# Optimization experiments

Hardware: AMD Instinct MI355X
Metric: run time of the kernel (lower is better)

The kernel has to match this reference:

```python
import jax, jax.numpy as jnp
import numpy as np

N = 10000       # nodes
E = 320000      # edges (before self-loops)
IN = 16         # in_channels


def _p(key, shape, scale=0.1):
    return jax.random.normal(key, shape, jnp.float32) * scale


def setup_inputs() -> dict:
    key = jax.random.key(0)
    ks = jax.random.split(key, 26)
    d = {}
    d["x"] = jax.random.normal(ks[0], (N, IN), jnp.float32)
    d["edge_index"] = jax.random.randint(ks[1], (2, E), 0, N, jnp.int32)
    d["JetRawPt"] = jax.random.normal(ks[2], (N, 1), jnp.float32)
    # conv1: GATConv(16 -> 32, heads=8)
    d["W1"] = _p(ks[3], (IN, 8 * 32)); d["a1s"] = _p(ks[4], (8, 32)); d["a1d"] = _p(ks[5], (8, 32)); d["b1"] = jnp.zeros((256,), jnp.float32)
    # conv2: GATConv(256 -> 32, heads=8)
    d["W2"] = _p(ks[6], (256, 8 * 32)); d["a2s"] = _p(ks[7], (8, 32)); d["a2d"] = _p(ks[8], (8, 32)); d["b2"] = jnp.zeros((256,), jnp.float32)
    # conv3: GATConv(256 -> 64, heads=12)
    d["W3"] = _p(ks[9], (256, 12 * 64)); d["a3s"] = _p(ks[10], (12, 64)); d["a3d"] = _p(ks[11], (12, 64)); d["b3"] = jnp.zeros((768,), jnp.float32)
    # linear_final: 256+256+768=1280 -> 1
    d["Wf"] = _p(ks[12], (1280, 1)); d["bf"] = jnp.zeros((1,), jnp.float32)
    # MLP: (16+1)->128->64->1
    d["M1w"] = _p(ks[13], (IN + 1, 128)); d["M1b"] = jnp.zeros((128,), jnp.float32)
    d["M2w"] = _p(ks[14], (128, 64)); d["M2b"] = jnp.zeros((64,), jnp.float32)
    d["M3w"] = _p(ks[15], (64, 1)); d["M3b"] = jnp.zeros((1,), jnp.float32)
    return d


def gat_layer(x, src, dst, W, a_s, a_d, b, H, C):
    # PyG GATConv (eval mode, self-loops already appended to src/dst)
    h = (x @ W).reshape(-1, H, C)                      # [N, H, C]
    al = jnp.sum(h * a_s, axis=-1)                     # [N, H] src-side score
    ar = jnp.sum(h * a_d, axis=-1)                     # [N, H] dst-side score
    e = jax.nn.leaky_relu(al[src] + ar[dst], 0.2)      # [Etot, H]
    m = jax.ops.segment_max(e, dst, num_segments=N)    # segment softmax over incoming edges
    ex = jnp.exp(e - m[dst])
    s = jax.ops.segment_sum(ex, dst, num_segments=N)
    alpha = ex / s[dst]                                # [Etot, H]
    out = jax.ops.segment_sum(h[src] * alpha[:, :, None], dst, num_segments=N)  # [N, H, C]
    return out.reshape(-1, H * C) + b


def reference(x, edge_index, JetRawPt, W1, a1s, a1d, b1, W2, a2s, a2d, b2,
              W3, a3s, a3d, b3, Wf, bf, M1w, M1b, M2w, M2b, M3w, M3b):
    loops = jnp.arange(N, dtype=edge_index.dtype)
    src = jnp.concatenate([edge_index[0], loops])
    dst = jnp.concatenate([edge_index[1], loops])
    x1 = jax.nn.relu(gat_layer(x, src, dst, W1, a1s, a1d, b1, 8, 32))
    x2 = jax.nn.relu(gat_layer(x1, src, dst, W2, a2s, a2d, b2, 8, 32))
    x3 = jax.nn.relu(gat_layer(x2, src, dst, W3, a3s, a3d, b3, 12, 64))
    xc = jnp.concatenate([x1, x2, x3], axis=1)         # [N, 1280]
    out1 = jax.nn.sigmoid(xc @ Wf + bf)                # [N, 1]
    xm = jnp.concatenate([x, out1], axis=1)            # [N, 17]
    h = jax.nn.relu(xm @ M1w + M1b)
    h = jax.nn.relu(h @ M2w + M2b)
    out2 = jax.nn.sigmoid(h @ M3w + M3b)               # [N, 1]
    return (out1, out2)
```

## Files before the change

### kernel.cpp

```cpp
#include <hip/hip_runtime.h>
#include <math.h>


typedef unsigned short bf16_t;
typedef __attribute__((ext_vector_type(8))) short bf16x8;
typedef __attribute__((ext_vector_type(4))) float f32x4;

__device__ inline float bf2f(bf16_t u) {
    union { unsigned int i; float f; } v; v.i = ((unsigned int)u) << 16; return v.f;
}
__device__ inline float u2f(unsigned int x) {
    union { unsigned int i; float f; } v; v.i = x; return v.f;
}
__device__ inline bf16_t f2bf(float f) {
    union { float f; unsigned int i; } v; v.f = f;
    unsigned int r = v.i + 0x7FFF + ((v.i >> 16) & 1);
    return (bf16_t)(r >> 16);
}


__global__ void zero_i32(int* p, int n) {
    int i = blockIdx.x * blockDim.x + threadIdx.x;
    if (i < n) p[i] = 0;
}

__global__ void count_edges(const int* __restrict__ ei, int E, int Nn,
                            int* __restrict__ counts) {
    int e = blockIdx.x * blockDim.x + threadIdx.x;
    if (e >= E + Nn) return;
    int dst = (e < E) ? ei[E + e] : (e - E);
    atomicAdd(&counts[dst], 1);
}

__global__ __launch_bounds__(1024) void scan_rowptr(const int* __restrict__ counts,
                                                    int* __restrict__ rowptr, int n) {
    const int IPT = (n + 1023) / 1024;
    int t = threadIdx.x;
    int base = t * IPT;
    int loc[16];
    int run = 0;
#pragma unroll
    for (int i = 0; i < 16; i++) {
        if (i >= IPT) break;
        int idx = base + i;
        int v = (idx < n) ? counts[idx] : 0;
        loc[i] = run;
        run += v;
    }
    int lane = t & 63, wid = t >> 6;
    int v = run;
    for (int off = 1; off < 64; off <<= 1) {
        int u = __shfl_up(v, off, 64);
        if (lane >= off) v += u;
    }
    __shared__ int wsum[16];
    __shared__ int woff[16];
    if (lane == 63) wsum[wid] = v;
    __syncthreads();
    if (t == 0) { int s = 0; for (int i = 0; i < 16; i++) { woff[i] = s; s += wsum[i]; } }
    __syncthreads();
    int excl = v - run + woff[wid];
#pragma unroll
    for (int i = 0; i < 16; i++) {
        if (i >= IPT) break;
        int idx = base + i;
        if (idx < n) rowptr[idx] = excl + loc[i];
    }
    if (t == 1023) rowptr[n] = excl + run;
}

__global__ void fill_edges(const int* __restrict__ ei, int E, int Nn,
                           const int* __restrict__ rowptr, int* __restrict__ cursor,
                           int* __restrict__ edge_src) {
    int e = blockIdx.x * blockDim.x + threadIdx.x;
    if (e >= E + Nn) return;
    int src, dst;
    if (e < E) { src = ei[e]; dst = ei[E + e]; }
    else       { src = e - E; dst = src; }
    int pos = atomicAdd(&cursor[dst], 1);
    edge_src[rowptr[dst] + pos] = src;
}

__global__ __launch_bounds__(256) void transpose_cast2(const float* __restrict__ W2,
                                                       bf16_t* __restrict__ Wt2,
                                                       const float* __restrict__ W3,
                                                       bf16_t* __restrict__ Wt3) {
    __shared__ float tile[16][17];
    const float* W; bf16_t* Wt; int Nc, n0;
    if (blockIdx.y < 16) { W = W2; Wt = Wt2; Nc = 256; n0 = blockIdx.y * 16; }
    else                 { W = W3; Wt = Wt3; Nc = 768; n0 = (blockIdx.y - 16) * 16; }
    int k0 = blockIdx.x * 16;
    int tx = threadIdx.x & 15, ty = threadIdx.x >> 4;
    tile[ty][tx] = W[(size_t)(k0 + ty) * Nc + n0 + tx];
    __syncthreads();
    Wt[(size_t)(n0 + ty) * 256 + k0 + tx] = f2bf(tile[tx][ty]);
}

__global__ __launch_bounds__(256) void gemm_f32_sc(const float* __restrict__ A,
                                                   const float* __restrict__ B,
                                                   bf16_t* __restrict__ Cm,
                                                   const float* __restrict__ a_s,
                                                   const float* __restrict__ a_d,
                                                   float* __restrict__ al,
                                                   float* __restrict__ ar,
                                                   int M, int K, int Nc, int H) {
    __shared__ float As[16][64];
    __shared__ float Bs[16][64];
    int t  = threadIdx.x;
    int tx = t & 15, ty = t >> 4;
    int row0 = blockIdx.y * 64, col0 = blockIdx.x * 64;
    int a_r = t >> 2, a_c = (t & 3) * 4;
    int b_r = t >> 4, b_c = (t & 15) * 4;

    float acc[4][4];
#pragma unroll
    for (int i = 0; i < 4; i++)
#pragma unroll
        for (int j = 0; j < 4; j++) acc[i][j] = 0.f;

    for (int kt = 0; kt < K; kt += 16) {
        float4 av = make_float4(0.f, 0.f, 0.f, 0.f);
        int gr = row0 + a_r;
        if (gr < M) av = *(const float4*)(A + (size_t)gr * K + kt + a_c);
        As[a_c + 0][a_r] = av.x;
        As[a_c + 1][a_r] = av.y;
        As[a_c + 2][a_r] = av.z;
        As[a_c + 3][a_r] = av.w;
        float4 bv = *(const float4*)(B + (size_t)(kt + b_r) * Nc + col0 + b_c);
        *(float4*)&Bs[b_r][b_c] = bv;
        __syncthreads();
#pragma unroll
        for (int k = 0; k < 16; k++) {
            float4 a4 = *(const float4*)&As[k][ty * 4];
            float4 b4 = *(const float4*)&Bs[k][tx * 4];
            float aa[4] = {a4.x, a4.y, a4.z, a4.w};
            float bb[4] = {b4.x, b4.y, b4.z, b4.w};
#pragma unroll
            for (int i = 0; i < 4; i++)
#pragma unroll
                for (int j = 0; j < 4; j++) acc[i][j] += aa[i] * bb[j];
        }
        __syncthreads();
    }
    float4 asv = *(const float4*)(a_s + col0 + tx * 4);
    float4 adv = *(const float4*)(a_d + col0 + tx * 4);
#pragma unroll
    for (int i = 0; i < 4; i++) {
        int gr = row0 + ty * 4 + i;
        float sa = acc[i][0] * asv.x + acc[i][1] * asv.y + acc[i][2] * asv.z + acc[i][3] * asv.w;
        float sd = acc[i][0] * adv.x + acc[i][1] * adv.y + acc[i][2] * adv.z + acc[i][3] * adv.w;
#pragma unroll
        for (int off = 4; off > 0; off >>= 1) {
            sa += __shfl_xor(sa, off, 64);
            sd += __shfl_xor(sd, off, 64);
        }
        if ((tx == 0 || tx == 8) && gr < M) {
            int h = (col0 >> 5) + (tx >> 3);
            al[gr * H + h] = sa;
            ar[gr * H + h] = sd;
        }
        if (gr < M) {
            ushort4 v;
            v.x = f2bf(acc[i][0]); v.y = f2bf(acc[i][1]);
            v.z = f2bf(acc[i][2]); v.w = f2bf(acc[i][3]);
            *(ushort4*)(Cm + (size_t)gr * Nc + col0 + tx * 4) = v;
        }
    }
}

template <int C_>
__global__ __launch_bounds__(256) void gemm_mfma_sc(const bf16_t* __restrict__ A,
                                                    const bf16_t* __restrict__ Bt,
                                                    bf16_t* __restrict__ Cm,
                                                    const float* __restrict__ a_s,
                                                    const float* __restrict__ a_d,
                                                    float* __restrict__ al,
                                                    float* __restrict__ ar,
                                                    int M, int K, int Nc, int H) {
    int wave = threadIdx.x >> 6, lane = threadIdx.x & 63;
    int quad = lane >> 4, l16 = lane & 15;
    int m0 = blockIdx.y * 128 + wave * 32;
    int n0 = blockIdx.x * 64;

    f32x4 acc[2][4];
    f32x4 z = {0.f, 0.f, 0.f, 0.f};
#pragma unroll
    for (int i = 0; i < 2; i++)
#pragma unroll
        for (int j = 0; j < 4; j++) acc[i][j] = z;

    int r0 = m0 + l16;       if (r0 >= M) r0 = M - 1;
    int r1 = m0 + 16 + l16;  if (r1 >= M) r1 = M - 1;
    const bf16_t* Ap0 = A + (size_t)r0 * K + quad * 8;
    const bf16_t* Ap1 = A + (size_t)r1 * K + quad * 8;
    const bf16_t* Bp0 = Bt + (size_t)(n0 + 0  + l16) * K + quad * 8;
    const bf16_t* Bp1 = Bt + (size_t)(n0 + 16 + l16) * K + quad * 8;
    const bf16_t* Bp2 = Bt + (size_t)(n0 + 32 + l16) * K + quad * 8;
    const bf16_t* Bp3 = Bt + (size_t)(n0 + 48 + l16) * K + quad * 8;

    for (int kt = 0; kt < K; kt += 32) {
        bf16x8 a0 = *(const bf16x8*)(Ap0 + kt);
        bf16x8 a1 = *(const bf16x8*)(Ap1 + kt);
        bf16x8 b0 = *(const bf16x8*)(Bp0 + kt);
        bf16x8 b1 = *(const bf16x8*)(Bp1 + kt);
        bf16x8 b2 = *(const bf16x8*)(Bp2 + kt);
        bf16x8 b3 = *(const bf16x8*)(Bp3 + kt);
        acc[0][0] = __builtin_amdgcn_mfma_f32_16x16x32_bf16(a0, b0, acc[0][0], 0, 0, 0);
        acc[1][0] = __builtin_amdgcn_mfma_f32_16x16x32_bf16(a1, b0, acc[1][0], 0, 0, 0);
        acc[0][1] = __builtin_amdgcn_mfma_f32_16x16x32_bf16(a0, b1, acc[0][1], 0, 0, 0);
        acc[1][1] = __builtin_amdgcn_mfma_f32_16x16x32_bf16(a1, b1, acc[1][1], 0, 0, 0);
        acc[0][2] = __builtin_amdgcn_mfma_f32_16x16x32_bf16(a0, b2, acc[0][2], 0, 0, 0);
        acc[1][2] = __builtin_amdgcn_mfma_f32_16x16x32_bf16(a1, b2, acc[1][2], 0, 0, 0);
        acc[0][3] = __builtin_amdgcn_mfma_f32_16x16x32_bf16(a0, b3, acc[0][3], 0, 0, 0);
        acc[1][3] = __builtin_amdgcn_mfma_f32_16x16x32_bf16(a1, b3, acc[1][3], 0, 0, 0);
    }

    float asv[4], adv[4];
#pragma unroll
    for (int j = 0; j < 4; j++) {
        asv[j] = a_s[n0 + j * 16 + l16];
        adv[j] = a_d[n0 + j * 16 + l16];
    }
#pragma unroll
    for (int i = 0; i < 2; i++)
#pragma unroll
        for (int r = 0; r < 4; r++) {
            int gr = m0 + i * 16 + quad * 4 + r;
            if (C_ == 64) {
                float sa = acc[i][0][r] * asv[0] + acc[i][1][r] * asv[1]
                         + acc[i][2][r] * asv[2] + acc[i][3][r] * asv[3];
                float sd = acc[i][0][r] * adv[0] + acc[i][1][r] * adv[1]
                         + acc[i][2][r] * adv[2] + acc[i][3][r] * adv[3];
#pragma unroll
                for (int off = 8; off > 0; off >>= 1) {
                    sa += __shfl_xor(sa, off, 64);
                    sd += __shfl_xor(sd, off, 64);
                }
                if (l16 == 0 && gr < M) {
                    int h = n0 >> 6;
                    al[gr * H + h] = sa;
                    ar[gr * H + h] = sd;
                }
            } else {
                float saA = acc[i][0][r] * asv[0] + acc[i][1][r] * asv[1];
                float saB = acc[i][2][r] * asv[2] + acc[i][3][r] * asv[3];
                float sdA = acc[i][0][r] * adv[0] + acc[i][1][r] * adv[1];
                float sdB = acc[i][2][r] * adv[2] + acc[i][3][r] * adv[3];
#pragma unroll
                for (int off = 8; off > 0; off >>= 1) {
                    saA += __shfl_xor(saA, off, 64);
                    saB += __shfl_xor(saB, off, 64);
                    sdA += __shfl_xor(sdA, off, 64);
                    sdB += __shfl_xor(sdB, off, 64);
                }
                if (l16 == 0 && gr < M) {
                    int h = n0 >> 5;
                    al[gr * H + h]     = saA;
                    ar[gr * H + h]     = sdA;
                    al[gr * H + h + 1] = saB;
                    ar[gr * H + h + 1] = sdB;
                }
            }
        }
#pragma unroll
    for (int i = 0; i < 2; i++)
#pragma unroll
        for (int j = 0; j < 4; j++)
#pragma unroll
            for (int r = 0; r < 4; r++) {
                int gr = m0 + i * 16 + quad * 4 + r;
                if (gr < M) Cm[(size_t)gr * Nc + n0 + j * 16 + l16] = f2bf(acc[i][j][r]);
            }
}

template <int H>
__global__ __launch_bounds__(256) void alpha_node(const float* __restrict__ al,
                                                  const float* __restrict__ ar,
                                                  const int* __restrict__ rowptr,
                                                  const int* __restrict__ esrc,
                                                  float* __restrict__ alpha,
                                                  int n, int Etot) {
    int node = (blockIdx.x * blockDim.x + threadIdx.x) >> 6;
    if (node >= n) return;
    int lane = threadIdx.x & 63;

    float arv[H];
#pragma unroll
    for (int h4 = 0; h4 < H; h4 += 4) {
        float4 t = *(const float4*)(ar + (size_t)node * H + h4);
        arv[h4] = t.x; arv[h4 + 1] = t.y; arv[h4 + 2] = t.z; arv[h4 + 3] = t.w;
    }
    int beg = rowptr[node], end = rowptr[node + 1];
    float p0[H], p1[H], s[H];
#pragma unroll
    for (int h = 0; h < H; h++) { p0[h] = 0.f; p1[h] = 0.f; s[h] = 0.f; }

    int j0 = beg + lane;
    if (j0 < end) {
        const float* alr = al + (size_t)esrc[j0] * H;
#pragma unroll
        for (int h4 = 0; h4 < H; h4 += 4) {
            float4 t = *(const float4*)(alr + h4);
            float e;
            e = t.x + arv[h4];     e = fmaxf(e, 0.2f * e); p0[h4]     = __expf(fminf(e, 60.f));
            e = t.y + arv[h4 + 1]; e = fmaxf(e, 0.2f * e); p0[h4 + 1] = __expf(fminf(e, 60.f));
            e = t.z + arv[h4 + 2]; e = fmaxf(e, 0.2f * e); p0[h4 + 2] = __expf(fminf(e, 60.f));
            e = t.w + arv[h4 + 3]; e = fmaxf(e, 0.2f * e); p0[h4 + 3] = __expf(fminf(e, 60.f));
        }
#pragma unroll
        for (int h = 0; h < H; h++) s[h] += p0[h];
    }
    int j1 = j0 + 64;
    if (j1 < end) {
        const float* alr = al + (size_t)esrc[j1] * H;
#pragma unroll
        for (int h4 = 0; h4 < H; h4 += 4) {
            float4 t = *(const float4*)(alr + h4);
            float e;
            e = t.x + arv[h4];     e = fmaxf(e, 0.2f * e); p1[h4]     = __expf(fminf(e, 60.f));
            e = t.y + arv[h4 + 1]; e = fmaxf(e, 0.2f * e); p1[h4 + 1] = __expf(fminf(e, 60.f));
            e = t.z + arv[h4 + 2]; e = fmaxf(e, 0.2f * e); p1[h4 + 2] = __expf(fminf(e, 60.f));
            e = t.w + arv[h4 + 3]; e = fmaxf(e, 0.2f * e); p1[h4 + 3] = __expf(fminf(e, 60.f));
        }
#pragma unroll
        for (int h = 0; h < H; h++) s[h] += p1[h];
    }
    for (int j = j0 + 128; j < end; j += 64) {
        const float* alr = al + (size_t)esrc[j] * H;
#pragma unroll
        for (int h = 0; h < H; h++) {
            float e = alr[h] + arv[h];
            e = fmaxf(e, 0.2f * e);
            float p = __expf(fminf(e, 60.f));
            alpha[(size_t)h * Etot + j] = p;
            s[h] += p;
        }
    }
#pragma unroll
    for (int h = 0; h < H; h++) {
        float v = s[h];
#pragma unroll
        for (int off = 32; off > 0; off >>= 1) v += __shfl_xor(v, off, 64);
        s[h] = 1.f / v;
    }
    if (j0 < end) {
#pragma unroll
        for (int h = 0; h < H; h++) alpha[(size_t)h * Etot + j0] = p0[h] * s[h];
    }
    if (j1 < end) {
#pragma unroll
        for (int h = 0; h < H; h++) alpha[(size_t)h * Etot + j1] = p1[h] * s[h];
    }
    for (int j = j0 + 128; j < end; j += 64) {
#pragma unroll
        for (int h = 0; h < H; h++) alpha[(size_t)h * Etot + j] *= s[h];
    }
}

template <int HC_, int C>
__global__ __launch_bounds__(256) void gat_agg(
    const bf16_t* __restrict__ hbuf, const float* __restrict__ alpha,
    const int* __restrict__ rowptr, const int* __restrict__ esrc,
    const float* __restrict__ bias, bf16_t* __restrict__ outb,
    int n, int Etot, int nodeblocks) {
    int group = blockIdx.x / nodeblocks;
    int nb    = blockIdx.x - group * nodeblocks;
    int node  = nb * 4 + (threadIdx.x >> 6);
    if (node >= n) return;
    int lane = threadIdx.x & 63;
    int sub  = lane >> 4;
    int cl   = lane & 15;
    int gc   = group * 128 + cl * 8;
    int head = gc / C;
    const bf16_t* hb = hbuf + gc;
    const float*  ap = alpha + (size_t)head * Etot;

    float acc[8];
#pragma unroll
    for (int i = 0; i < 8; i++) acc[i] = 0.f;

    int beg = rowptr[node], end = rowptr[node + 1];
    int deg = end - beg;

    int e0 = 0, e1 = 0;
    {
        int i0 = beg + lane;
        if (i0 < end) e0 = esrc[i0];
        int i1 = beg + 64 + lane;
        if (i1 < end) e1 = esrc[i1];
    }
    int npre  = deg < 128 ? deg : 128;
    int nfull = npre >> 3;

    if (nfull > 0) {
        int s0 = __shfl(e0, sub, 64);
        int s1 = __shfl(e0, sub + 4, 64);
        float a0 = ap[beg + sub], a1 = ap[beg + sub + 4];
        bf16x8 u0 = *(const bf16x8*)(hb + (size_t)s0 * HC_);
        bf16x8 u1 = *(const bf16x8*)(hb + (size_t)s1 * HC_);
        for (int it = 1; it < nfull; ++it) {
            int kb = it * 8;
            int esel = (kb < 64) ? e0 : e1;
            int t0 = __shfl(esel, (kb + sub) & 63, 64);
            int t1 = __shfl(esel, (kb + sub + 4) & 63, 64);
            float b0v = ap[beg + kb + sub], b1v = ap[beg + kb + sub + 4];
            bf16x8 v0 = *(const bf16x8*)(hb + (size_t)t0 * HC_);
            bf16x8 v1 = *(const bf16x8*)(hb + (size_t)t1 * HC_);
            const unsigned int* d0 = (const unsigned int*)&u0;
            const unsigned int* d1 = (const unsigned int*)&u1;
#pragma unroll
            for (int i = 0; i < 4; i++) {
                acc[2 * i]     += a0 * u2f(d0[i] << 16);
                acc[2 * i + 1] += a0 * u2f(d0[i] & 0xffff0000u);
                acc[2 * i]     += a1 * u2f(d1[i] << 16);
                acc[2 * i + 1] += a1 * u2f(d1[i] & 0xffff0000u);
            }
            u0 = v0; u1 = v1; a0 = b0v; a1 = b1v;
        }
        const unsigned int* d0 = (const unsigned int*)&u0;
        const unsigned int* d1 = (const unsigned int*)&u1;
#pragma unroll
        for (int i = 0; i < 4; i++) {
            acc[2 * i]     += a0 * u2f(d0[i] << 16);
            acc[2 * i + 1] += a0 * u2f(d0[i] & 0xffff0000u);
            acc[2 * i]     += a1 * u2f(d1[i] << 16);
            acc[2 * i + 1] += a1 * u2f(d1[i] & 0xffff0000u);
        }
    }
    for (int j = beg + (nfull << 3) + sub; j < end; j += 4) {
        int s0 = esrc[j];
        float a0 = ap[j];
        bf16x8 u0 = *(const bf16x8*)(hb + (size_t)s0 * HC_);
        const unsigned int* d0 = (const unsigned int*)&u0;
#pragma unroll
        for (int i = 0; i < 4; i++) {
            acc[2 * i]     += a0 * u2f(d0[i] << 16);
            acc[2 * i + 1] += a0 * u2f(d0[i] & 0xffff0000u);
        }
    }
#pragma unroll
    for (int i = 0; i < 8; i++) {
        acc[i] += __shfl_xor(acc[i], 16, 64);
        acc[i] += __shfl_xor(acc[i], 32, 64);
    }
    if (sub == 0) {
        float4 b0 = *(const float4*)(bias + gc);
        float4 b1 = *(const float4*)(bias + gc + 4);
        float bb[8] = {b0.x, b0.y, b0.z, b0.w, b1.x, b1.y, b1.z, b1.w};
        bf16x8 outv;
        unsigned short* ov = (unsigned short*)&outv;
#pragma unroll
        for (int i = 0; i < 8; i++) ov[i] = f2bf(fmaxf(acc[i] + bb[i], 0.f));
        *(bf16x8*)(outb + (size_t)node * HC_ + gc) = outv;
    }
}

__global__ __launch_bounds__(256) void head_fused(
    const float* __restrict__ x, const bf16_t* __restrict__ x1b,
    const bf16_t* __restrict__ x2b, const bf16_t* __restrict__ x3b,
    const float* __restrict__ Wf, const float* __restrict__ bfc,
    const float* __restrict__ M1w, const float* __restrict__ M1b,
    const float* __restrict__ M2w, const float* __restrict__ M2b,
    const float* __restrict__ M3w, const float* __restrict__ M3b,
    float* __restrict__ out1, float* __restrict__ out2, int n) {
    __shared__ float h1s[4][128];
    int w    = threadIdx.x >> 6;
    int lane = threadIdx.x & 63;
    int node = blockIdx.x * 4 + w;
    bool valid = node < n;
    int nd = valid ? node : 0;

    float s = 0.f;
    {
        ushort4 u = *(const ushort4*)(x1b + (size_t)nd * 256 + lane * 4);
        const float* wv = Wf + lane * 4;
        s += bf2f(u.x) * wv[0] + bf2f(u.y) * wv[1] + bf2f(u.z) * wv[2] + bf2f(u.w) * wv[3];
    }
    {
        ushort4 u = *(const ushort4*)(x2b + (size_t)nd * 256 + lane * 4);
        const float* wv = Wf + 256 + lane * 4;
        s += bf2f(u.x) * wv[0] + bf2f(u.y) * wv[1] + bf2f(u.z) * wv[2] + bf2f(u.w) * wv[3];
    }
#pragma unroll
    for (int i = 0; i < 3; i++) {
        int k = i * 256 + lane * 4;
        ushort4 u = *(const ushort4*)(x3b + (size_t)nd * 768 + k);
        const float* wv = Wf + 512 + k;
        s += bf2f(u.x) * wv[0] + bf2f(u.y) * wv[1] + bf2f(u.z) * wv[2] + bf2f(u.w) * wv[3];
    }
#pragma unroll
    for (int off = 32; off > 0; off >>= 1) s += __shfl_xor(s, off, 64);
    float so = 1.f / (1.f + __expf(-(s + bfc[0])));
    if (lane == 0 && valid) out1[node] = so;

    float xm[17];
#pragma unroll
    for (int k = 0; k < 16; k++) xm[k] = x[nd * 16 + k];
    xm[16] = so;

    float a0 = M1b[lane], a1 = M1b[lane + 64];
#pragma unroll
    for (int k = 0; k < 17; k++) {
        a0 += xm[k] * M1w[k * 128 + lane];
        a1 += xm[k] * M1w[k * 128 + lane + 64];
    }
    h1s[w][lane]      = fmaxf(a0, 0.f);
    h1s[w][lane + 64] = fmaxf(a1, 0.f);
    __syncthreads();

    float b0 = M2b[lane];
#pragma unroll 16
    for (int k = 0; k < 128; k++) b0 += h1s[w][k] * M2w[k * 64 + lane];
    b0 = fmaxf(b0, 0.f);

    float p = b0 * M3w[lane];
#pragma unroll
    for (int off = 32; off > 0; off >>= 1) p += __shfl_xor(p, off, 64);
    if (lane == 0 && valid) out2[node] = 1.f / (1.f + __expf(-(p + M3b[0])));
}

extern "C" void kernel_launch(void* const* d_in, const int* in_sizes, int n_in,
                              void* d_out, int out_size, void* d_ws, size_t ws_size,
                              hipStream_t stream) {
    const float* x   = (const float*)d_in[0];
    const int*   ei  = (const int*)d_in[1];
    const float* W1  = (const float*)d_in[3];
    const float* a1s = (const float*)d_in[4];
    const float* a1d = (const float*)d_in[5];
    const float* b1  = (const float*)d_in[6];
    const float* W2  = (const float*)d_in[7];
    const float* a2s = (const float*)d_in[8];
    const float* a2d = (const float*)d_in[9];
    const float* b2  = (const float*)d_in[10];
    const float* W3  = (const float*)d_in[11];
    const float* a3s = (const float*)d_in[12];
    const float* a3d = (const float*)d_in[13];
    const float* b3  = (const float*)d_in[14];
    const float* Wf  = (const float*)d_in[15];
    const float* bf  = (const float*)d_in[16];
    const float* M1w = (const float*)d_in[17];
    const float* M1b = (const float*)d_in[18];
    const float* M2w = (const float*)d_in[19];
    const float* M2b = (const float*)d_in[20];
    const float* M3w = (const float*)d_in[21];
    const float* M3b = (const float*)d_in[22];

    const int N = in_sizes[0] / 16;
    const int E = in_sizes[1] / 2;
    const int Etot = E + N;

    char* base = (char*)d_ws;
    size_t off = 0;
    auto carve = [&](size_t bytes) {
        char* p = base + off;
        off = (off + bytes + 255) & ~(size_t)255;
        return p;
    };
    bf16_t* hbuf   = (bf16_t*)carve((size_t)N * 768 * 2);
    bf16_t* x1b    = (bf16_t*)carve((size_t)N * 256 * 2);
    bf16_t* x2b    = (bf16_t*)carve((size_t)N * 256 * 2);
    bf16_t* x3b    = (bf16_t*)carve((size_t)N * 768 * 2);
    bf16_t* Wt2    = (bf16_t*)carve((size_t)256 * 256 * 2);
    bf16_t* Wt3    = (bf16_t*)carve((size_t)256 * 768 * 2);
    float*  al     = (float*)carve((size_t)N * 12 * 4);
    float*  ar     = (float*)carve((size_t)N * 12 * 4);
    float*  alphab = (float*)carve((size_t)Etot * 12 * 4);
    int*    rowptr = (int*)carve((size_t)(N + 1) * 4);
    int*    cnt2   = (int*)carve((size_t)(2 * N) * 4);
    int*    counts = cnt2;
    int*    cursor = cnt2 + N;
    int*    esrc   = (int*)carve((size_t)Etot * 4);
    (void)ws_size;

    float* out1 = (float*)d_out;
    float* out2 = (float*)d_out + N;

    const int TB = 256;
    int eb = (Etot + TB - 1) / TB;
    int nodeblocks = (N + 3) / 4;

    zero_i32<<<(2 * N + TB - 1) / TB, TB, 0, stream>>>(cnt2, 2 * N);
    count_edges<<<eb, TB, 0, stream>>>(ei, E, N, counts);
    scan_rowptr<<<1, 1024, 0, stream>>>(counts, rowptr, N);
    fill_edges<<<eb, TB, 0, stream>>>(ei, E, N, rowptr, cursor, esrc);
    transpose_cast2<<<dim3(16, 64), TB, 0, stream>>>(W2, Wt2, W3, Wt3);

    gemm_f32_sc<<<dim3(4, (N + 63) / 64), TB, 0, stream>>>(x, W1, hbuf, a1s, a1d, al, ar, N, 16, 256, 8);
    alpha_node<8><<<nodeblocks, TB, 0, stream>>>(al, ar, rowptr, esrc, alphab, N, Etot);
    gat_agg<256, 32><<<2 * nodeblocks, TB, 0, stream>>>(hbuf, alphab, rowptr, esrc, b1, x1b, N, Etot, nodeblocks);

    gemm_mfma_sc<32><<<dim3(4, (N + 127) / 128), TB, 0, stream>>>(x1b, Wt2, hbuf, a2s, a2d, al, ar, N, 256, 256, 8);
    alpha_node<8><<<nodeblocks, TB, 0, stream>>>(al, ar, rowptr, esrc, alphab, N, Etot);
    gat_agg<256, 32><<<2 * nodeblocks, TB, 0, stream>>>(hbuf, alphab, rowptr, esrc, b2, x2b, N, Etot, nodeblocks);

    gemm_mfma_sc<64><<<dim3(12, (N + 127) / 128), TB, 0, stream>>>(x2b, Wt3, hbuf, a3s, a3d, al, ar, N, 256, 768, 12);
    alpha_node<12><<<nodeblocks, TB, 0, stream>>>(al, ar, rowptr, esrc, alphab, N, Etot);
    gat_agg<768, 64><<<6 * nodeblocks, TB, 0, stream>>>(hbuf, alphab, rowptr, esrc, b3, x3b, N, Etot, nodeblocks);

    head_fused<<<nodeblocks, TB, 0, stream>>>(x, x1b, x2b, x3b, Wf, bf,
                                              M1w, M1b, M2w, M2b, M3w, M3b, out1, out2, N);
}
```

Baseline: 335.1 us.

## Process two nodes per wavefront in alpha_node, pack aggregation FMAs, use memset

alpha_node now gives each node a 32-lane half wavefront instead of a full 64-lane wavefront. With about 33 edges per node, this cuts idle lanes and halves the grid, though high-degree nodes now loop more. gat_agg accumulates into float2 vectors, aiming for packed FP32 FMA instructions. The zero-fill kernel is replaced by hipMemsetAsync.

```diff
diff --git a/kernel.cpp b/kernel.cpp
--- a/kernel.cpp
+++ b/kernel.cpp
@@ -5,6 +5,7 @@
 typedef unsigned short bf16_t;
 typedef __attribute__((ext_vector_type(8))) short bf16x8;
 typedef __attribute__((ext_vector_type(4))) float f32x4;
+typedef __attribute__((ext_vector_type(2))) float f32x2;
 
 __device__ inline float bf2f(bf16_t u) {
     union { unsigned int i; float f; } v; v.i = ((unsigned int)u) << 16; return v.f;
@@ -18,11 +19,6 @@
     return (bf16_t)(r >> 16);
 }
 
-
-__global__ void zero_i32(int* p, int n) {
-    int i = blockIdx.x * blockDim.x + threadIdx.x;
-    if (i < n) p[i] = 0;
-}
 
 __global__ void count_edges(const int* __restrict__ ei, int E, int Nn,
                             int* __restrict__ counts) {
@@ -280,9 +276,11 @@
                                                   const int* __restrict__ esrc,
                                                   float* __restrict__ alpha,
                                                   int n, int Etot) {
-    int node = (blockIdx.x * blockDim.x + threadIdx.x) >> 6;
+    int pair = (blockIdx.x * blockDim.x + threadIdx.x) >> 6;
+    int lane = threadIdx.x & 63;
+    int node = pair * 2 + (lane >> 5);
     if (node >= n) return;
-    int lane = threadIdx.x & 63;
+    int lane32 = lane & 31;
 
     float arv[H];
 #pragma unroll
@@ -295,7 +293,7 @@
 #pragma unroll
     for (int h = 0; h < H; h++) { p0[h] = 0.f; p1[h] = 0.f; s[h] = 0.f; }
 
-    int j0 = beg + lane;
+    int j0 = beg + lane32;
     if (j0 < end) {
         const float* alr = al + (size_t)esrc[j0] * H;
 #pragma unroll
@@ -310,7 +308,7 @@
 #pragma unroll
         for (int h = 0; h < H; h++) s[h] += p0[h];
     }
-    int j1 = j0 + 64;
+    int j1 = j0 + 32;
     if (j1 < end) {
         const float* alr = al + (size_t)esrc[j1] * H;
 #pragma unroll
@@ -325,7 +323,7 @@
 #pragma unroll
         for (int h = 0; h < H; h++) s[h] += p1[h];
     }
-    for (int j = j0 + 128; j < end; j += 64) {
+    for (int j = j0 + 64; j < end; j += 32) {
         const float* alr = al + (size_t)esrc[j] * H;
 #pragma unroll
         for (int h = 0; h < H; h++) {
@@ -340,7 +338,7 @@
     for (int h = 0; h < H; h++) {
         float v = s[h];
 #pragma unroll
-        for (int off = 32; off > 0; off >>= 1) v += __shfl_xor(v, off, 64);
+        for (int off = 16; off > 0; off >>= 1) v += __shfl_xor(v, off, 64);
         s[h] = 1.f / v;
     }
     if (j0 < end) {
@@ -351,7 +349,7 @@
 #pragma unroll
         for (int h = 0; h < H; h++) alpha[(size_t)h * Etot + j1] = p1[h] * s[h];
     }
-    for (int j = j0 + 128; j < end; j += 64) {
+    for (int j = j0 + 64; j < end; j += 32) {
 #pragma unroll
         for (int h = 0; h < H; h++) alpha[(size_t)h * Etot + j] *= s[h];
     }
@@ -375,9 +373,10 @@
     const bf16_t* hb = hbuf + gc;
     const float*  ap = alpha + (size_t)head * Etot;
 
-    float acc[8];
-#pragma unroll
-    for (int i = 0; i < 8; i++) acc[i] = 0.f;
+    f32x2 acc2[4];
+    f32x2 z2 = {0.f, 0.f};
+#pragma unroll
+    for (int i = 0; i < 4; i++) acc2[i] = z2;
 
     int beg = rowptr[node], end = rowptr[node + 1];
     int deg = end - beg;
@@ -408,23 +407,25 @@
             bf16x8 v1 = *(const bf16x8*)(hb + (size_t)t1 * HC_);
             const unsigned int* d0 = (const unsigned int*)&u0;
             const unsigned int* d1 = (const unsigned int*)&u1;
+            f32x2 a0v = {a0, a0}, a1v = {a1, a1};
 #pragma unroll
             for (int i = 0; i < 4; i++) {
-                acc[2 * i]     += a0 * u2f(d0[i] << 16);
-                acc[2 * i + 1] += a0 * u2f(d0[i] & 0xffff0000u);
-                acc[2 * i]     += a1 * u2f(d1[i] << 16);
-                acc[2 * i + 1] += a1 * u2f(d1[i] & 0xffff0000u);
+                f32x2 w0 = {u2f(d0[i] << 16), u2f(d0[i] & 0xffff0000u)};
+                f32x2 w1 = {u2f(d1[i] << 16), u2f(d1[i] & 0xffff0000u)};
+                acc2[i] += a0v * w0;
+                acc2[i] += a1v * w1;
             }
             u0 = v0; u1 = v1; a0 = b0v; a1 = b1v;
         }
         const unsigned int* d0 = (const unsigned int*)&u0;
         const unsigned int* d1 = (const unsigned int*)&u1;
+        f32x2 a0v = {a0, a0}, a1v = {a1, a1};
 #pragma unroll
         for (int i = 0; i < 4; i++) {
-            acc[2 * i]     += a0 * u2f(d0[i] << 16);
-            acc[2 * i + 1] += a0 * u2f(d0[i] & 0xffff0000u);
-            acc[2 * i]     += a1 * u2f(d1[i] << 16);
-            acc[2 * i + 1] += a1 * u2f(d1[i] & 0xffff0000u);
+            f32x2 w0 = {u2f(d0[i] << 16), u2f(d0[i] & 0xffff0000u)};
+            f32x2 w1 = {u2f(d1[i] << 16), u2f(d1[i] & 0xffff0000u)};
+            acc2[i] += a0v * w0;
+            acc2[i] += a1v * w1;
         }
     }
     for (int j = beg + (nfull << 3) + sub; j < end; j += 4) {
@@ -432,12 +433,15 @@
         float a0 = ap[j];
         bf16x8 u0 = *(const bf16x8*)(hb + (size_t)s0 * HC_);
         const unsigned int* d0 = (const unsigned int*)&u0;
+        f32x2 a0v = {a0, a0};
 #pragma unroll
         for (int i = 0; i < 4; i++) {
-            acc[2 * i]     += a0 * u2f(d0[i] << 16);
-            acc[2 * i + 1] += a0 * u2f(d0[i] & 0xffff0000u);
-        }
-    }
+            f32x2 w0 = {u2f(d0[i] << 16), u2f(d0[i] & 0xffff0000u)};
+            acc2[i] += a0v * w0;
+        }
+    }
+    float acc[8] = {acc2[0].x, acc2[0].y, acc2[1].x, acc2[1].y,
+                    acc2[2].x, acc2[2].y, acc2[3].x, acc2[3].y};
 #pragma unroll
     for (int i = 0; i < 8; i++) {
         acc[i] += __shfl_xor(acc[i], 16, 64);
@@ -578,23 +582,24 @@
     const int TB = 256;
     int eb = (Etot + TB - 1) / TB;
     int nodeblocks = (N + 3) / 4;
-
-    zero_i32<<<(2 * N + TB - 1) / TB, TB, 0, stream>>>(cnt2, 2 * N);
+    int alphablocks = (N + 7) / 8;
+
+    hipMemsetAsync(cnt2, 0, (size_t)(2 * N) * 4, stream);
     count_edges<<<eb, TB, 0, stream>>>(ei, E, N, counts);
     scan_rowptr<<<1, 1024, 0, stream>>>(counts, rowptr, N);
     fill_edges<<<eb, TB, 0, stream>>>(ei, E, N, rowptr, cursor, esrc);
     transpose_cast2<<<dim3(16, 64), TB, 0, stream>>>(W2, Wt2, W3, Wt3);
 
     gemm_f32_sc<<<dim3(4, (N + 63) / 64), TB, 0, stream>>>(x, W1, hbuf, a1s, a1d, al, ar, N, 16, 256, 8);
-    alpha_node<8><<<nodeblocks, TB, 0, stream>>>(al, ar, rowptr, esrc, alphab, N, Etot);
+    alpha_node<8><<<alphablocks, TB, 0, stream>>>(al, ar, rowptr, esrc, alphab, N, Etot);
     gat_agg<256, 32><<<2 * nodeblocks, TB, 0, stream>>>(hbuf, alphab, rowptr, esrc, b1, x1b, N, Etot, nodeblocks);
 
     gemm_mfma_sc<32><<<dim3(4, (N + 127) / 128), TB, 0, stream>>>(x1b, Wt2, hbuf, a2s, a2d, al, ar, N, 256, 256, 8);
-    alpha_node<8><<<nodeblocks, TB, 0, stream>>>(al, ar, rowptr, esrc, alphab, N, Etot);
+    alpha_node<8><<<alphablocks, TB, 0, stream>>>(al, ar, rowptr, esrc, alphab, N, Etot);
     gat_agg<256, 32><<<2 * nodeblocks, TB, 0, stream>>>(hbuf, alphab, rowptr, esrc, b2, x2b, N, Etot, nodeblocks);
 
     gemm_mfma_sc<64><<<dim3(12, (N + 127) / 128), TB, 0, stream>>>(x2b, Wt3, hbuf, a3s, a3d, al, ar, N, 256, 768, 12);
-    alpha_node<12><<<nodeblocks, TB, 0, stream>>>(al, ar, rowptr, esrc, alphab, N, Etot);
+    alpha_node<12><<<alphablocks, TB, 0, stream>>>(al, ar, rowptr, esrc, alphab, N, Etot);
     gat_agg<768, 64><<<6 * nodeblocks, TB, 0, stream>>>(hbuf, alphab, rowptr, esrc, b3, x3b, N, Etot, nodeblocks);
 
     head_fused<<<nodeblocks, TB, 0, stream>>>(x, x1b, x2b, x3b, Wf, bf,
```

Result: faster. 327.4 us (-2.3%).
